# Kernel optimization log

Measured on AMD Instinct MI355X. Metric: run time of the kernel, lower is better.

## Reference

```python
import jax, jax.numpy as jnp
import numpy as np

B, S, D, H = 2, 2048, 1024, 16
DH = D // H
LN_EPS = 1e-12


def setup_inputs() -> dict:
    key = jax.random.key(0)
    ks = jax.random.split(key, 11)
    s = 0.02
    return {
        "hidden_states": jax.random.normal(ks[0], (B, S, D), dtype=jnp.float32),
        "Wq": jax.random.normal(ks[1], (D, D), dtype=jnp.float32) * s,
        "bq": jnp.zeros((D,), jnp.float32),
        "Wk": jax.random.normal(ks[2], (D, D), dtype=jnp.float32) * s,
        "bk": jnp.zeros((D,), jnp.float32),
        "Wv": jax.random.normal(ks[3], (D, D), dtype=jnp.float32) * s,
        "bv": jnp.zeros((D,), jnp.float32),
        "Wd": jax.random.normal(ks[4], (D, D), dtype=jnp.float32) * s,  # torch Linear weight [out,in]
        "bd": jnp.zeros((D,), jnp.float32),
        "ln_g": jnp.ones((D,), jnp.float32),
        "ln_b": jnp.zeros((D,), jnp.float32),
    }


def reference(hidden_states, Wq, bq, Wk, bk, Wv, bv, Wd, bd, ln_g, ln_b):
    x = hidden_states  # [B,S,D]
    # torch Linear: y = x @ W.T + b
    def heads(y):
        return y.reshape(B, S, H, DH).transpose(0, 2, 1, 3)  # [B,H,S,DH]

    q = heads(x @ Wq.T + bq)
    k = heads(x @ Wk.T + bk)
    v = heads(x @ Wv.T + bv)

    scores = jnp.einsum('bhsd,bhtd->bhst', q, k) / jnp.sqrt(jnp.float32(DH))
    probs = jax.nn.softmax(scores, axis=-1)  # [B,H,S,S]
    ctx = jnp.einsum('bhst,bhtd->bshd', probs, v)  # [B,S,H,DH]

    # fused output projection: einsum('bfnd,ndh->bfh') with w = Wd.T reshaped
    w = Wd.T.reshape(H, DH, D)
    proj = jnp.einsum('bfnd,ndh->bfh', ctx, w) + bd  # [B,S,D]

    mu = jnp.mean(proj, axis=-1, keepdims=True)
    var = jnp.var(proj, axis=-1, keepdims=True)
    out = (proj - mu) / jnp.sqrt(var + LN_EPS) * ln_g + ln_b
    return out
```

## Files before the change

### kernel.cpp

```cpp
#include <hip/hip_runtime.h>

#define HD 16
#define DHEAD 64
#define DMODEL 1024
#define BB 2
#define SS 2048
#define MTOT (BB*SS)
#define LOG2E 1.44269504f

typedef float f32x4 __attribute__((ext_vector_type(4)));
typedef float f32x16 __attribute__((ext_vector_type(16)));
typedef __bf16 bf16x8 __attribute__((ext_vector_type(8)));
typedef unsigned short u16x8 __attribute__((ext_vector_type(8)));
typedef unsigned int u32x2 __attribute__((ext_vector_type(2)));
typedef unsigned int u32x4 __attribute__((ext_vector_type(4)));

__device__ __forceinline__ unsigned short f2bf(float f) {
    unsigned int u = __builtin_bit_cast(unsigned int, f);
    unsigned int r = (u + 0x7fffu + ((u >> 16) & 1u)) >> 16;
    return (unsigned short)r;
}

__device__ __forceinline__ bf16x8 ld8(const unsigned short* p) {
    u16x8 v = *reinterpret_cast<const u16x8*>(p);
    return __builtin_bit_cast(bf16x8, v);
}

__device__ __forceinline__ void gload_lds16b(const char* g, char* l) {
    __builtin_amdgcn_global_load_lds(
        (const __attribute__((address_space(1))) void*)g,
        (__attribute__((address_space(3))) void*)l, 16, 0, 0);
}

__device__ __forceinline__ unsigned cvt_pk_bf16(float lo, float hi) {
    unsigned r;
    asm("v_cvt_pk_bf16_f32 %0, %1, %2" : "=v"(r) : "v"(lo), "v"(hi));
    return r;
}

__global__ __launch_bounds__(256) void cvt_all(
    const float* __restrict__ x,
    const float* __restrict__ w0, const float* __restrict__ w1,
    const float* __restrict__ w2, const float* __restrict__ w3,
    unsigned short* __restrict__ xb,
    unsigned short* __restrict__ o0, unsigned short* __restrict__ o1,
    unsigned short* __restrict__ o2, unsigned short* __restrict__ o3) {
    int y = blockIdx.y;
    const float* in;
    unsigned short* out;
    int idx;
    if (y < 4) {
        in  = (y == 0) ? w0 : (y == 1) ? w1 : (y == 2) ? w2 : w3;
        out = (y == 0) ? o0 : (y == 1) ? o1 : (y == 2) ? o2 : o3;
        idx = blockIdx.x * 256 + threadIdx.x;
    } else {
        in  = x;
        out = xb;
        idx = ((y - 4) * 1024 + blockIdx.x) * 256 + threadIdx.x;
    }
    float4 v = reinterpret_cast<const float4*>(in)[idx];
    ushort4 o;
    o.x = f2bf(v.x); o.y = f2bf(v.y); o.z = f2bf(v.z); o.w = f2bf(v.w);
    reinterpret_cast<ushort4*>(out)[idx] = o;
}

__global__ __launch_bounds__(256, 2) void gemm_qkv(
    const unsigned short* __restrict__ xb,
    const unsigned short* __restrict__ Wqb, const unsigned short* __restrict__ Wkb,
    const unsigned short* __restrict__ Wvb,
    const float* __restrict__ bq, const float* __restrict__ bk, const float* __restrict__ bv,
    unsigned short* __restrict__ Qo, unsigned short* __restrict__ Ko, unsigned short* __restrict__ VTo) {
    __shared__ unsigned short Als[2][8192];
    __shared__ unsigned short Bls[2][8192];
    int L = blockIdx.x;
    int wg = (L & 7) * 96 + (L >> 3);
    int z = wg >> 8, rem = wg & 255;
    int n0 = (rem & 7) * 128, m0 = (rem >> 3) * 128;
    const unsigned short* Bm = (z == 0) ? Wqb : (z == 1) ? Wkb : Wvb;
    const float* bias = (z == 0) ? bq : (z == 1) ? bk : bv;

    int t = threadIdx.x, wv = t >> 6, lane = t & 63;
    int q5 = lane & 31, hi = lane >> 5;
    int wm = wv >> 1, wn = wv & 1;
    const char* Ac = (const char*)xb;
    const char* Bc = (const char*)Bm;

    auto stage = [&](int bf, int k0) {
#pragma unroll
        for (int i = 0; i < 4; ++i) {
            int c = t + 256 * i;
            int kr = c >> 3, kc = ((c & 7) << 4) ^ ((kr & 7) << 4);
            gload_lds16b(Ac + ((size_t)(m0 + kr) * DMODEL + k0) * 2 + kc, (char*)&Als[bf][0] + c * 16);
        }
#pragma unroll
        for (int i = 0; i < 4; ++i) {
            int c = t + 256 * i;
            int kr = c >> 3, kc = ((c & 7) << 4) ^ ((kr & 7) << 4);
            gload_lds16b(Bc + ((size_t)(n0 + kr) * DMODEL + k0) * 2 + kc, (char*)&Bls[bf][0] + c * 16);
        }
    };

    f32x16 acc[2][2];
#pragma unroll
    for (int fm = 0; fm < 2; ++fm)
#pragma unroll
        for (int fn = 0; fn < 2; ++fn) acc[fm][fn] = (f32x16)0.f;

    stage(0, 0);
    int buf = 0;
    for (int k0 = 0; k0 < DMODEL; k0 += 64) {
        __builtin_amdgcn_s_barrier();
        if (k0 + 64 < DMODEL) {
            stage(buf ^ 1, k0 + 64);
            asm volatile("s_waitcnt vmcnt(8)" ::: "memory");
        } else {
            asm volatile("s_waitcnt vmcnt(0)" ::: "memory");
        }
        __builtin_amdgcn_sched_barrier(0);
        __builtin_amdgcn_s_barrier();
        __builtin_amdgcn_sched_barrier(0);

        const char* als = (const char*)&Als[buf][0];
        const char* bls = (const char*)&Bls[buf][0];
        __builtin_amdgcn_s_setprio(1);
#pragma unroll
        for (int ks = 0; ks < 4; ++ks) {
            int kb = ks * 32 + hi * 16;
            bf16x8 af[2], bfr[2];
#pragma unroll
            for (int fm = 0; fm < 2; ++fm) {
                int row = wm * 64 + fm * 32 + q5;
                af[fm] = *reinterpret_cast<const bf16x8*>(als + row * 128 + (kb ^ ((row & 7) << 4)));
            }
#pragma unroll
            for (int fn = 0; fn < 2; ++fn) {
                int row = wn * 64 + fn * 32 + q5;
                bfr[fn] = *reinterpret_cast<const bf16x8*>(bls + row * 128 + (kb ^ ((row & 7) << 4)));
            }
#pragma unroll
            for (int fm = 0; fm < 2; ++fm)
#pragma unroll
                for (int fn = 0; fn < 2; ++fn)
                    acc[fm][fn] = __builtin_amdgcn_mfma_f32_32x32x16_bf16(af[fm], bfr[fn], acc[fm][fn], 0, 0, 0);
        }
        __builtin_amdgcn_s_setprio(0);
        buf ^= 1;
    }

    float scale = (z == 0) ? (0.125f * LOG2E) : 1.0f;
    int b = m0 >> 11;
#pragma unroll
    for (int fm = 0; fm < 2; ++fm) {
#pragma unroll
        for (int fn = 0; fn < 2; ++fn) {
            int col = n0 + wn * 64 + fn * 32 + q5;
            int h = col >> 6, dh = col & 63;
            float bi = bias[col];
            if (z == 2) {
#pragma unroll
                for (int rq = 0; rq < 4; ++rq) {
                    int s0 = ((m0 + wm * 64 + fm * 32 + 8 * rq + 4 * hi) & 2047);
                    ushort4 pk;
                    pk.x = f2bf(acc[fm][fn][4 * rq + 0] + bi);
                    pk.y = f2bf(acc[fm][fn][4 * rq + 1] + bi);
                    pk.z = f2bf(acc[fm][fn][4 * rq + 2] + bi);
                    pk.w = f2bf(acc[fm][fn][4 * rq + 3] + bi);
                    *reinterpret_cast<ushort4*>(&VTo[((size_t)((b * HD + h) * DHEAD + dh)) * SS + s0]) = pk;
                }
            } else {
                unsigned short* o = (z == 0) ? Qo : Ko;
#pragma unroll
                for (int r = 0; r < 16; ++r) {
                    int s = (m0 + wm * 64 + fm * 32 + (r & 3) + 8 * (r >> 2) + 4 * hi) & 2047;
                    o[((size_t)((b * HD + h) * SS + s)) * DHEAD + dh] = f2bf((acc[fm][fn][r] + bi) * scale);
                }
            }
        }
    }
}

__global__ __launch_bounds__(256, 4) void attn_kernel(
    const unsigned short* __restrict__ Qb, const unsigned short* __restrict__ Kb,
    const unsigned short* __restrict__ VTb, unsigned short* __restrict__ ctxo) {
    __shared__ unsigned short Kls[2][4096];
    __shared__ unsigned short Vls[2][4096];
    int L = blockIdx.x + (int)gridDim.x * blockIdx.y;
    int wg = (L & 7) * 64 + (L >> 3);
    int q0 = (wg & 15) * 128;
    int bh = wg >> 4;
    int t = threadIdx.x, wv = t >> 6, lane = t & 63;
    int q5 = lane & 31, hi = lane >> 5;
    const unsigned short* Qh  = Qb  + (size_t)bh * SS * DHEAD;
    const char* Khc  = (const char*)(Kb  + (size_t)bh * SS * DHEAD);
    const char* VThc = (const char*)(VTb + (size_t)bh * DHEAD * SS);
    int qr = q0 + wv * 32;

    bf16x8 qf[4];
#pragma unroll
    for (int m = 0; m < 4; ++m)
        qf[m] = ld8(&Qh[(size_t)(qr + q5) * DHEAD + m * 16 + hi * 8]);

    const __bf16 one_bf = (__bf16)1.0f;
    bf16x8 ones8 = {one_bf, one_bf, one_bf, one_bf, one_bf, one_bf, one_bf, one_bf};

    f32x16 oo[2];
    oo[0] = (f32x16)0.f; oo[1] = (f32x16)0.f;
    f32x16 ls = (f32x16)0.f;
    float mrun = 0.f;

    auto stage = [&](int buf, int t0) {
#pragma unroll
        for (int i = 0; i < 2; ++i) {
            int c = t + 256 * i;
            int kr = c >> 3, kc = ((c & 7) << 4) ^ ((kr & 7) << 4);
            gload_lds16b(Khc + (size_t)(t0 + kr) * 128 + kc, (char*)&Kls[buf][0] + c * 16);
        }
#pragma unroll
        for (int i = 0; i < 2; ++i) {
            int c = t + 256 * i;
            int vr = c >> 3, vc = ((c & 7) << 4) ^ ((vr & 7) << 4);
            gload_lds16b(VThc + ((size_t)vr * SS + t0) * 2 + vc, (char*)&Vls[buf][0] + c * 16);
        }
    };

    stage(0, 0);
    int buf = 0;

    for (int t0 = 0; t0 < SS; t0 += 64) {
        __builtin_amdgcn_s_barrier();
        if (t0 + 64 < SS) {
            stage(buf ^ 1, t0 + 64);
            asm volatile("s_waitcnt vmcnt(4)" ::: "memory");
        } else {
            asm volatile("s_waitcnt vmcnt(0)" ::: "memory");
        }
        __builtin_amdgcn_sched_barrier(0);
        __builtin_amdgcn_s_barrier();
        __builtin_amdgcn_sched_barrier(0);

        const char* kls = (const char*)&Kls[buf][0];
        const char* vls = (const char*)&Vls[buf][0];

        f32x16 sc[2];
        __builtin_amdgcn_s_setprio(1);
#pragma unroll
        for (int tb = 0; tb < 2; ++tb) {
            int row = tb * 32 + q5;
            int rsw = (row & 7) << 4;
            f32x16 s = (f32x16)0.f;
#pragma unroll
            for (int m = 0; m < 4; ++m) {
                bf16x8 kf = *reinterpret_cast<const bf16x8*>(kls + row * 128 + ((m * 32 + hi * 16) ^ rsw));
                s = __builtin_amdgcn_mfma_f32_32x32x16_bf16(kf, qf[m], s, 0, 0, 0);
            }
            sc[tb] = s;
        }
        __builtin_amdgcn_s_setprio(0);

        float mx[16];
#pragma unroll
        for (int r = 0; r < 16; ++r) mx[r] = fmaxf(sc[0][r], sc[1][r]);
#pragma unroll
        for (int st = 8; st; st >>= 1)
#pragma unroll
            for (int r = 0; r < st; ++r) mx[r] = fmaxf(mx[r], mx[r + st]);
        float lm = mx[0];

        if (__any(lm > mrun + 8.f)) {
            u32x2 sw = __builtin_amdgcn_permlane32_swap(__builtin_bit_cast(unsigned, lm),
                                                        __builtin_bit_cast(unsigned, lm), false, false);
            float rowmax = fmaxf(__builtin_bit_cast(float, sw[0]), __builtin_bit_cast(float, sw[1]));
            float mn = fmaxf(mrun, rowmax);
            float al = exp2f(mrun - mn);
            mrun = mn;
#pragma unroll
            for (int r = 0; r < 16; ++r) {
                float alr = __shfl(al, (r & 3) + 8 * (r >> 2) + 4 * hi);
                oo[0][r] *= alr; oo[1][r] *= alr; ls[r] *= alr;
            }
        }

#pragma unroll
        for (int tb = 0; tb < 2; ++tb)
#pragma unroll
            for (int r = 0; r < 16; ++r)
                sc[tb][r] = exp2f(sc[tb][r] - mrun);

        u32x4 paw[4];
#pragma unroll
        for (int tb = 0; tb < 2; ++tb)
#pragma unroll
            for (int u2 = 0; u2 < 2; ++u2)
#pragma unroll
                for (int e = 0; e < 2; ++e) {
                    unsigned wd = cvt_pk_bf16(sc[tb][8 * u2 + 2 * e], sc[tb][8 * u2 + 2 * e + 1]);
                    unsigned ws = cvt_pk_bf16(sc[tb][8 * u2 + 4 + 2 * e], sc[tb][8 * u2 + 4 + 2 * e + 1]);
                    u32x2 rr = __builtin_amdgcn_permlane32_swap(wd, ws, false, false);
                    paw[tb * 2 + u2][e] = rr[0];
                    paw[tb * 2 + u2][2 + e] = rr[1];
                }

        __builtin_amdgcn_s_setprio(1);
#pragma unroll
        for (int dblk = 0; dblk < 2; ++dblk) {
            int row = dblk * 32 + q5;
            int rsw = (row & 7) << 4;
#pragma unroll
            for (int ks = 0; ks < 4; ++ks) {
                bf16x8 vf = *reinterpret_cast<const bf16x8*>(
                    vls + row * 128 + ((ks * 32 + hi * 16) ^ rsw));
                oo[dblk] = __builtin_amdgcn_mfma_f32_32x32x16_bf16(
                    __builtin_bit_cast(bf16x8, paw[ks]), vf, oo[dblk], 0, 0, 0);
            }
        }
#pragma unroll
        for (int ks = 0; ks < 4; ++ks)
            ls = __builtin_amdgcn_mfma_f32_32x32x16_bf16(
                __builtin_bit_cast(bf16x8, paw[ks]), ones8, ls, 0, 0, 0);
        __builtin_amdgcn_s_setprio(0);
        buf ^= 1;
    }

    int b = bh >> 4, h = bh & 15;
#pragma unroll
    for (int r = 0; r < 16; ++r) {
        float invr = 1.f / ls[r];
        int qrel = (r & 3) + 8 * (r >> 2) + 4 * hi;
        int s = qr + qrel;
        size_t base = ((size_t)(b * SS + s)) * DMODEL + h * DHEAD;
        ctxo[base + q5]      = f2bf(oo[0][r] * invr);
        ctxo[base + 32 + q5] = f2bf(oo[1][r] * invr);
    }
}

__global__ __launch_bounds__(256, 2) void gemm_proj(
    const unsigned short* __restrict__ ctxb, const unsigned short* __restrict__ Wdb,
    const float* __restrict__ bd, float* __restrict__ proj) {
    __shared__ unsigned short Als[2][8192];
    __shared__ unsigned short Bls[2][4096];
    int L = blockIdx.x;
    int wg = (L & 7) * 64 + (L >> 3);
    int n0 = (wg & 15) * 64, m0 = (wg >> 4) * 128;

    int t = threadIdx.x, wv = t >> 6, lane = t & 63;
    int q5 = lane & 31, hi = lane >> 5;
    int wm = wv >> 1, wn = wv & 1;
    const char* Ac = (const char*)ctxb;
    const char* Bc = (const char*)Wdb;

    auto stage = [&](int bf, int k0) {
#pragma unroll
        for (int i = 0; i < 4; ++i) {
            int c = t + 256 * i;
            int kr = c >> 3, kc = ((c & 7) << 4) ^ ((kr & 7) << 4);
            gload_lds16b(Ac + ((size_t)(m0 + kr) * DMODEL + k0) * 2 + kc, (char*)&Als[bf][0] + c * 16);
        }
#pragma unroll
        for (int i = 0; i < 2; ++i) {
            int c = t + 256 * i;
            int kr = c >> 3, kc = ((c & 7) << 4) ^ ((kr & 7) << 4);
            gload_lds16b(Bc + ((size_t)(n0 + kr) * DMODEL + k0) * 2 + kc, (char*)&Bls[bf][0] + c * 16);
        }
    };

    f32x16 acc[2];
    acc[0] = (f32x16)0.f; acc[1] = (f32x16)0.f;

    stage(0, 0);
    int buf = 0;
    for (int k0 = 0; k0 < DMODEL; k0 += 64) {
        __builtin_amdgcn_s_barrier();
        if (k0 + 64 < DMODEL) {
            stage(buf ^ 1, k0 + 64);
            asm volatile("s_waitcnt vmcnt(6)" ::: "memory");
        } else {
            asm volatile("s_waitcnt vmcnt(0)" ::: "memory");
        }
        __builtin_amdgcn_sched_barrier(0);
        __builtin_amdgcn_s_barrier();
        __builtin_amdgcn_sched_barrier(0);

        const char* als = (const char*)&Als[buf][0];
        const char* bls = (const char*)&Bls[buf][0];
        __builtin_amdgcn_s_setprio(1);
#pragma unroll
        for (int ks = 0; ks < 4; ++ks) {
            int kb = ks * 32 + hi * 16;
            bf16x8 af[2], bfr;
#pragma unroll
            for (int fm = 0; fm < 2; ++fm) {
                int row = wm * 64 + fm * 32 + q5;
                af[fm] = *reinterpret_cast<const bf16x8*>(als + row * 128 + (kb ^ ((row & 7) << 4)));
            }
            {
                int row = wn * 32 + q5;
                bfr = *reinterpret_cast<const bf16x8*>(bls + row * 128 + (kb ^ ((row & 7) << 4)));
            }
#pragma unroll
            for (int fm = 0; fm < 2; ++fm)
                acc[fm] = __builtin_amdgcn_mfma_f32_32x32x16_bf16(af[fm], bfr, acc[fm], 0, 0, 0);
        }
        __builtin_amdgcn_s_setprio(0);
        buf ^= 1;
    }

    int col = n0 + wn * 32 + q5;
    float bi = bd[col];
#pragma unroll
    for (int fm = 0; fm < 2; ++fm)
#pragma unroll
        for (int r = 0; r < 16; ++r) {
            int row = m0 + wm * 64 + fm * 32 + (r & 3) + 8 * (r >> 2) + 4 * hi;
            proj[(size_t)row * DMODEL + col] = acc[fm][r] + bi;
        }
}

__global__ __launch_bounds__(256) void ln_kernel(const float* __restrict__ proj,
                                                 const float* __restrict__ g,
                                                 const float* __restrict__ bv,
                                                 float* __restrict__ out) {
    int row = blockIdx.x, t = threadIdx.x;
    float4 v = reinterpret_cast<const float4*>(proj + (size_t)row * DMODEL)[t];
    float s  = v.x + v.y + v.z + v.w;
    float s2 = v.x * v.x + v.y * v.y + v.z * v.z + v.w * v.w;
#pragma unroll
    for (int m = 1; m < 64; m <<= 1) { s += __shfl_xor(s, m); s2 += __shfl_xor(s2, m); }
    __shared__ float red[8];
    int wv = t >> 6, lane = t & 63;
    if (lane == 0) { red[wv] = s; red[wv + 4] = s2; }
    __syncthreads();
    s  = red[0] + red[1] + red[2] + red[3];
    s2 = red[4] + red[5] + red[6] + red[7];
    float mu  = s * (1.f / 1024.f);
    float var = s2 * (1.f / 1024.f) - mu * mu;
    float inv = rsqrtf(var + 1e-12f);
    float4 gv = reinterpret_cast<const float4*>(g)[t];
    float4 bb = reinterpret_cast<const float4*>(bv)[t];
    float4 ov;
    ov.x = (v.x - mu) * inv * gv.x + bb.x;
    ov.y = (v.y - mu) * inv * gv.y + bb.y;
    ov.z = (v.z - mu) * inv * gv.z + bb.z;
    ov.w = (v.w - mu) * inv * gv.w + bb.w;
    reinterpret_cast<float4*>(out + (size_t)row * DMODEL)[t] = ov;
}

extern "C" void kernel_launch(void* const* d_in, const int* in_sizes, int n_in,
                              void* d_out, int out_size, void* d_ws, size_t ws_size,
                              hipStream_t stream) {
    const float* x   = (const float*)d_in[0];
    const float* Wq  = (const float*)d_in[1];
    const float* bq  = (const float*)d_in[2];
    const float* Wk  = (const float*)d_in[3];
    const float* bk  = (const float*)d_in[4];
    const float* Wv  = (const float*)d_in[5];
    const float* bv  = (const float*)d_in[6];
    const float* Wd  = (const float*)d_in[7];
    const float* bd  = (const float*)d_in[8];
    const float* lng = (const float*)d_in[9];
    const float* lnb = (const float*)d_in[10];

    char* ws = (char*)d_ws;
    unsigned short* xb   = (unsigned short*)(ws);
    unsigned short* Wqb  = (unsigned short*)(ws + (8u  << 20));
    unsigned short* Wkb  = (unsigned short*)(ws + (10u << 20));
    unsigned short* Wvb  = (unsigned short*)(ws + (12u << 20));
    unsigned short* Wdb  = (unsigned short*)(ws + (14u << 20));
    unsigned short* Qb   = (unsigned short*)(ws + (16u << 20));
    unsigned short* Kb   = (unsigned short*)(ws + (24u << 20));
    unsigned short* VTb  = (unsigned short*)(ws + (32u << 20));
    unsigned short* ctxb = (unsigned short*)(ws + (40u << 20));
    float* proj = (float*)(ws + (16u << 20));

    cvt_all<<<dim3(1024, 8), 256, 0, stream>>>(x, Wq, Wk, Wv, Wd, xb, Wqb, Wkb, Wvb, Wdb);
    gemm_qkv<<<768, 256, 0, stream>>>(xb, Wqb, Wkb, Wvb, bq, bk, bv, Qb, Kb, VTb);
    attn_kernel<<<dim3(16, 32), 256, 0, stream>>>(Qb, Kb, VTb, ctxb);
    gemm_proj<<<512, 256, 0, stream>>>(ctxb, Wdb, bd, proj);
    ln_kernel<<<4096, 256, 0, stream>>>(proj, lng, lnb, (float*)d_out);
}
```

Baseline: 148.1 us.

## Deepen attention K/V pipeline to four LDS stages with single barrier

Replaces the double-buffered K/V staging in the attention kernel with a 4-slot ring buffer that keeps three tiles in flight. Each iteration now uses one barrier instead of two. The vmcnt waits are adjusted to the deeper prefetch. The idea is to hide more global load latency, at the cost of doubling LDS use to 64KB per block and lowering the launch-bounds occupancy hint from 4 to 2 blocks.

Result: faster. 139.0 us (-6.1%).

```diff
diff --git a/kernel.cpp b/kernel.cpp
--- a/kernel.cpp
+++ b/kernel.cpp
@@ -179,11 +179,10 @@
     }
 }
 
-__global__ __launch_bounds__(256, 4) void attn_kernel(
+__global__ __launch_bounds__(256, 2) void attn_kernel(
     const unsigned short* __restrict__ Qb, const unsigned short* __restrict__ Kb,
     const unsigned short* __restrict__ VTb, unsigned short* __restrict__ ctxo) {
-    __shared__ unsigned short Kls[2][4096];
-    __shared__ unsigned short Vls[2][4096];
+    __shared__ char smem[4][16384];
     int L = blockIdx.x + (int)gridDim.x * blockIdx.y;
     int wg = (L & 7) * 64 + (L >> 3);
     int q0 = (wg & 15) * 128;
@@ -208,38 +207,38 @@
     f32x16 ls = (f32x16)0.f;
     float mrun = 0.f;
 
-    auto stage = [&](int buf, int t0) {
+    auto stage = [&](int ph) {
+        char* kb = smem[ph & 3];
+        char* vb = kb + 8192;
+        int t0 = ph * 64;
 #pragma unroll
         for (int i = 0; i < 2; ++i) {
             int c = t + 256 * i;
             int kr = c >> 3, kc = ((c & 7) << 4) ^ ((kr & 7) << 4);
-            gload_lds16b(Khc + (size_t)(t0 + kr) * 128 + kc, (char*)&Kls[buf][0] + c * 16);
+            gload_lds16b(Khc + (size_t)(t0 + kr) * 128 + kc, kb + c * 16);
         }
 #pragma unroll
         for (int i = 0; i < 2; ++i) {
             int c = t + 256 * i;
             int vr = c >> 3, vc = ((c & 7) << 4) ^ ((vr & 7) << 4);
-            gload_lds16b(VThc + ((size_t)vr * SS + t0) * 2 + vc, (char*)&Vls[buf][0] + c * 16);
+            gload_lds16b(VThc + ((size_t)vr * SS + t0) * 2 + vc, vb + c * 16);
         }
     };
 
-    stage(0, 0);
-    int buf = 0;
-
-    for (int t0 = 0; t0 < SS; t0 += 64) {
+    stage(0); stage(1); stage(2);
+
+    for (int ph = 0; ph < 32; ++ph) {
+        if (ph < 30)      asm volatile("s_waitcnt vmcnt(8)" ::: "memory");
+        else if (ph == 30) asm volatile("s_waitcnt vmcnt(4)" ::: "memory");
+        else              asm volatile("s_waitcnt vmcnt(0)" ::: "memory");
+        __builtin_amdgcn_sched_barrier(0);
         __builtin_amdgcn_s_barrier();
-        if (t0 + 64 < SS) {
-            stage(buf ^ 1, t0 + 64);
-            asm volatile("s_waitcnt vmcnt(4)" ::: "memory");
-        } else {
-            asm volatile("s_waitcnt vmcnt(0)" ::: "memory");
-        }
-        __builtin_amdgcn_sched_barrier(0);
-        __builtin_amdgcn_s_barrier();
-        __builtin_amdgcn_sched_barrier(0);
-
-        const char* kls = (const char*)&Kls[buf][0];
-        const char* vls = (const char*)&Vls[buf][0];
+        __builtin_amdgcn_sched_barrier(0);
+
+        if (ph + 3 < 32) stage(ph + 3);
+
+        const char* kls = smem[ph & 3];
+        const char* vls = kls + 8192;
 
         f32x16 sc[2];
         __builtin_amdgcn_s_setprio(1);
@@ -318,7 +317,6 @@
             ls = __builtin_amdgcn_mfma_f32_32x32x16_bf16(
                 __builtin_bit_cast(bf16x8, paw[ks]), ones8, ls, 0, 0, 0);
         __builtin_amdgcn_s_setprio(0);
-        buf ^= 1;
     }
 
     int b = bh >> 4, h = bh & 15;
```
